# Performance work log

Measured on AMD Instinct MI355X. Metric: run time of the kernel, lower is better.

## Reference

```python
import math
import jax, jax.numpy as jnp
import numpy as np

HEADS = 8
D_MODEL = 256


def positional_encoding_2d(c, h, w):
    # faithful port of wzlxjtu/PositionalEncoding2D
    d = c // 2
    div_term = jnp.exp(jnp.arange(0.0, d, 2, dtype=jnp.float32) * (-(math.log(10000.0) / d)))  # [d//2? no: d/2 entries -> d//2]
    pos_w = jnp.arange(0.0, w, dtype=jnp.float32)[:, None] * div_term  # [w, d//2]
    pos_h = jnp.arange(0.0, h, dtype=jnp.float32)[:, None] * div_term  # [h, d//2]
    pe = jnp.zeros((c, h, w), dtype=jnp.float32)
    sw = jnp.broadcast_to(jnp.sin(pos_w).T[:, None, :], (div_term.shape[0], h, w))
    cw = jnp.broadcast_to(jnp.cos(pos_w).T[:, None, :], (div_term.shape[0], h, w))
    sh = jnp.broadcast_to(jnp.sin(pos_h).T[:, :, None], (div_term.shape[0], h, w))
    ch = jnp.broadcast_to(jnp.cos(pos_h).T[:, :, None], (div_term.shape[0], h, w))
    pe = pe.at[0:d:2].set(sw)
    pe = pe.at[1:d:2].set(cw)
    pe = pe.at[d::2].set(sh)
    pe = pe.at[d + 1::2].set(ch)
    return pe


def setup_inputs() -> dict:
    key = jax.random.key(0)
    ks = jax.random.split(key, 9)
    b, c, h, w = 2, D_MODEL, 64, 64
    x = jax.random.normal(ks[0], (b, c, h, w), dtype=jnp.float32)
    s = 0.02
    Wq = jax.random.normal(ks[1], (c, c), dtype=jnp.float32) * s
    Wk = jax.random.normal(ks[2], (c, c), dtype=jnp.float32) * s
    Wv = jax.random.normal(ks[3], (c, c), dtype=jnp.float32) * s
    Wo = jax.random.normal(ks[4], (c, c), dtype=jnp.float32) * s
    bq = jax.random.normal(ks[5], (c,), dtype=jnp.float32) * s
    bk = jax.random.normal(ks[6], (c,), dtype=jnp.float32) * s
    bv = jax.random.normal(ks[7], (c,), dtype=jnp.float32) * s
    bo = jax.random.normal(ks[8], (c,), dtype=jnp.float32) * s
    return {"x": x, "Wq": Wq, "bq": bq, "Wk": Wk, "bk": bk,
            "Wv": Wv, "bv": bv, "Wo": Wo, "bo": bo}


def reference(x, Wq, bq, Wk, bk, Wv, bv, Wo, bo):
    b, c, h, w = x.shape
    dk = c // HEADS
    pe = positional_encoding_2d(c, h, w)
    x2 = x + pe[None]                                   # [b,c,h,w]
    tok = x2.reshape(b, c, h * w).transpose(0, 2, 1)    # [b,N,c]
    q = (tok @ Wq.T + bq).reshape(b, -1, HEADS, dk).transpose(0, 2, 1, 3)  # [b,H,N,dk]
    k = (tok @ Wk.T + bk).reshape(b, -1, HEADS, dk).transpose(0, 2, 1, 3)
    v = (tok @ Wv.T + bv).reshape(b, -1, HEADS, dk).transpose(0, 2, 1, 3)
    scores = jnp.einsum('bhnd,bhmd->bhnm', q, k) / math.sqrt(dk)  # [b,H,N,N]
    attn = jax.nn.softmax(scores, axis=-1)
    out = jnp.einsum('bhnm,bhmd->bhnd', attn, v)        # [b,H,N,dk]
    concat = out.transpose(0, 2, 1, 3).reshape(b, -1, c)  # [b,N,c]
    proj = concat @ Wo.T + bo                           # [b,N,c]
    return proj.transpose(0, 2, 1).reshape(b, c, h, w)
```

## Files before the change

### kernel.cpp

```cpp
#include <hip/hip_runtime.h>
#include <hip/hip_bf16.h>
#include <cstdint>

typedef float f32x4 __attribute__((ext_vector_type(4)));
typedef __bf16 bf16x8 __attribute__((ext_vector_type(8)));
typedef __bf16 bf16x2 __attribute__((ext_vector_type(2)));
typedef uint32_t uint2v __attribute__((ext_vector_type(2)));
typedef uint32_t uint4v __attribute__((ext_vector_type(4)));

#define MFMA_K32(A, B, C) __builtin_amdgcn_mfma_f32_16x16x32_bf16((A), (B), (C), 0, 0, 0)

#if __has_builtin(__builtin_amdgcn_exp2f)
#define EXP2(x) __builtin_amdgcn_exp2f(x)
#else
#define EXP2(x) exp2f(x)
#endif

static __device__ __forceinline__ uint16_t f2b(float f) {
    uint32_t u = __float_as_uint(f);
    uint32_t r = (u + 0x7fffu + ((u >> 16) & 1u)) >> 16;
    return (uint16_t)r;
}

static __device__ __forceinline__ uint32_t packbf(float a, float b) {
#if __has_builtin(__builtin_amdgcn_cvt_pk_bf16_f32)
    bf16x2 v = __builtin_amdgcn_cvt_pk_bf16_f32(a, b);
    return *(uint32_t*)&v;
#else
    uint32_t ua = __float_as_uint(a);
    ua += 0x7fffu + ((ua >> 16) & 1u);
    uint32_t ub = __float_as_uint(b);
    ub += 0x7fffu + ((ub >> 16) & 1u);
    return __builtin_amdgcn_perm(ub, ua, 0x07060302);
#endif
}

__global__ __launch_bounds__(256) void peadd(const float* __restrict__ x,
                                             uint16_t* __restrict__ tok) {
    __shared__ uint16_t T[64][65];
    int t = threadIdx.x, bid = blockIdx.x;
    int nt = bid & 63, ct = (bid >> 6) & 3, bb = bid >> 8;
    int n0 = nt << 6, c0 = ct << 6;
    int nl = t & 63, cq = t >> 6;
    int n = n0 + nl;
    int posh = n0 >> 6;
    float pf = (float)((c0 & 128) ? posh : nl);
#pragma unroll
    for (int p = 0; p < 16; ++p) {
        int cl = cq * 16 + p;
        int cc = c0 + cl;
        int i = (cc & 127) >> 1;
        float dt = __expf((float)(2 * i) * -0.07195578415606394f);
        float sv, cv;
        __sincosf(pf * dt, &sv, &cv);
        float pe = (cc & 1) ? cv : sv;
        T[cl][nl] = f2b(x[((size_t)(bb * 256 + cc) << 12) + n] + pe);
    }
    __syncthreads();
#pragma unroll
    for (int p = 0; p < 16; ++p) {
        int tl = cq * 16 + p;
        tok[(((size_t)(bb << 12) | (n0 + tl)) << 8) + c0 + nl] = T[nl][tl];
    }
}

__global__ __launch_bounds__(256) void qkv_gemm(const uint16_t* __restrict__ tok,
                                                const float* __restrict__ wqp,
                                                const float* __restrict__ wkp,
                                                const float* __restrict__ wvp,
                                                const float* __restrict__ bq,
                                                const float* __restrict__ bk,
                                                const float* __restrict__ bv,
                                                uint16_t* __restrict__ qo,
                                                uint16_t* __restrict__ ko,
                                                uint16_t* __restrict__ vo) {
    __shared__ __align__(16) uint16_t WS[64][264];
    int tid = threadIdx.x, wv = tid >> 6, lane = tid & 63;
    int c16 = lane & 15, quad = lane >> 4;
    int M0 = blockIdx.x * 64 + wv * 16;
    int O0 = blockIdx.y * 64;
    const uint16_t* arow = tok + (size_t)(M0 + c16) * 256;
    bf16x8 af[8];
#pragma unroll
    for (int kk = 0; kk < 8; ++kk) af[kk] = *(const bf16x8*)(arow + kk * 32 + quad * 8);
    f32x4 zero = {0.f, 0.f, 0.f, 0.f};
    int bb = M0 >> 12, n = (M0 + c16) & 4095;
    int srow = tid >> 5, sch = (tid & 31) << 3;
    for (int mat = 0; mat < 3; ++mat) {
        const float* Wg = ((mat == 0) ? wqp : (mat == 1) ? wkp : wvp) + (size_t)O0 * 256;
        __syncthreads();
#pragma unroll
        for (int p = 0; p < 8; ++p) {
            const float* src = Wg + (size_t)(p * 8 + srow) * 256 + sch;
            f32x4 lo = *(const f32x4*)(src);
            f32x4 hi = *(const f32x4*)(src + 4);
            uint4v pk;
            pk[0] = packbf(lo[0], lo[1]);
            pk[1] = packbf(lo[2], lo[3]);
            pk[2] = packbf(hi[0], hi[1]);
            pk[3] = packbf(hi[2], hi[3]);
            *(uint4v*)(&WS[p * 8 + srow][sch]) = pk;
        }
        __syncthreads();
        f32x4 acc[4] = {zero, zero, zero, zero};
#pragma unroll
        for (int kk = 0; kk < 8; ++kk) {
            int k0 = kk * 32 + quad * 8;
#pragma unroll
            for (int nb = 0; nb < 4; ++nb)
                acc[nb] = MFMA_K32(*(const bf16x8*)(&WS[nb * 16 + c16][k0]),
                                   af[kk], acc[nb]);
        }
        const float* bias = (mat == 0) ? bq : (mat == 1) ? bk : bv;
        if (mat < 2) {
            float scale = (mat == 0) ? 0.25505654134660127f : 1.0f;
            uint16_t* dst = (mat == 0) ? qo : ko;
#pragma unroll
            for (int nb = 0; nb < 4; ++nb) {
                int o = O0 + nb * 16 + quad * 4;
                f32x4 bi = *(const f32x4*)(bias + o);
                int h = o >> 5, dd = o & 31;
                uint2v pk;
                pk[0] = packbf((acc[nb][0] + bi[0]) * scale, (acc[nb][1] + bi[1]) * scale);
                pk[1] = packbf((acc[nb][2] + bi[2]) * scale, (acc[nb][3] + bi[3]) * scale);
                *(uint2v*)(dst + ((size_t)(bb * 8 + h) * 4096 + n) * 32 + dd) = pk;
            }
        } else {
#pragma unroll
            for (int nb = 0; nb < 4; ++nb)
#pragma unroll
                for (int r = 0; r < 4; ++r) {
                    int o = O0 + nb * 16 + quad * 4 + r;
                    vo[((size_t)(bb * 8 + (o >> 5)) * 32 + (o & 31)) * 4096 + n] =
                        f2b(acc[nb][r] + bias[o]);
                }
        }
    }
}

__global__ __launch_bounds__(512, 4) void flash(const uint16_t* __restrict__ qb,
                                                const uint16_t* __restrict__ kb,
                                                const uint16_t* __restrict__ vtb,
                                                uint16_t* __restrict__ concat) {
    __shared__ __align__(16) char smem[38912];
    int tid = threadIdx.x, wv = tid >> 6, lane = tid & 63;
    int c16 = lane & 15, quad = lane >> 4;
    int half = tid >> 8, t2 = tid & 255;
    int bh = blockIdx.y;
    int q0 = (blockIdx.x << 7) + (wv & 3) * 32;
    size_t base = (size_t)bh << 12;

    uint16_t* KT = (uint16_t*)(smem + half * 19456);
    uint16_t* VT = (uint16_t*)(smem + half * 19456 + 10240);

    const uint16_t* kgp = kb + (base + (size_t)half * 2048 + (t2 >> 2)) * 32 + (t2 & 3) * 8;
    const uint16_t* vgp = vtb + ((size_t)bh * 32 + (t2 >> 3)) * 4096 + half * 2048 + (t2 & 7) * 8;
    uint16_t* kls = KT + (t2 >> 2) * 40 + (t2 & 3) * 8;
    uint16_t* vls = VT + (t2 >> 3) * 72 + (t2 & 7) * 8;

    bf16x8 qf0 = *(const bf16x8*)(qb + (base + q0 + c16) * 32 + quad * 8);
    bf16x8 qf1 = *(const bf16x8*)(qb + (base + q0 + 16 + c16) * 32 + quad * 8);

    int rbase = ((c16 >> 2) << 3) + (c16 & 3);

    union { uint32_t u[4]; bf16x8 v; } onesu;
    onesu.u[0] = 0x3F803F80u; onesu.u[1] = 0x3F803F80u;
    onesu.u[2] = 0x3F803F80u; onesu.u[3] = 0x3F803F80u;
    bf16x8 ones = onesu.v;

    f32x4 zero = {0.f, 0.f, 0.f, 0.f};
    f32x4 o00 = zero, o01 = zero, o10 = zero, o11 = zero;
    f32x4 oS0 = zero, oS1 = zero;

    {
        bf16x8 kr = *(const bf16x8*)kgp;
        bf16x8 vr = *(const bf16x8*)vgp;
        *(bf16x8*)kls = kr;
        *(bf16x8*)vls = vr;
    }
    __syncthreads();

    for (int kt = 0; kt < 32; ++kt) {
        int cur = kt & 1;
        int kn = (kt + 1) & 31;
        bf16x8 kr = *(const bf16x8*)(kgp + (size_t)kn * 2048);
        bf16x8 vr = *(const bf16x8*)(vgp + kn * 64);
        const uint16_t* kfp = KT + cur * 2560 + rbase * 40 + quad * 8;
        const uint16_t* vfp = VT + cur * 2304 + c16 * 72 + quad * 8;
        bf16x8 kf[4], vA[2], vB[2];
        kf[0] = *(const bf16x8*)(kfp);
        kf[1] = *(const bf16x8*)(kfp + 160);
        kf[2] = *(const bf16x8*)(kfp + 1280);
        kf[3] = *(const bf16x8*)(kfp + 1440);
        vA[0] = *(const bf16x8*)(vfp);
        vA[1] = *(const bf16x8*)(vfp + 32);
        vB[0] = *(const bf16x8*)(vfp + 1152);
        vB[1] = *(const bf16x8*)(vfp + 1152 + 32);

        f32x4 s0[4], s1[4];
#pragma unroll
        for (int c = 0; c < 4; ++c) s0[c] = MFMA_K32(kf[c], qf0, zero);
#pragma unroll
        for (int c = 0; c < 4; ++c) s1[c] = MFMA_K32(kf[c], qf1, zero);

#pragma unroll
        for (int p = 0; p < 2; ++p) {
#pragma unroll
            for (int r = 0; r < 4; ++r) {
                s0[2 * p][r] = EXP2(s0[2 * p][r]);
                s0[2 * p + 1][r] = EXP2(s0[2 * p + 1][r]);
                s1[2 * p][r] = EXP2(s1[2 * p][r]);
                s1[2 * p + 1][r] = EXP2(s1[2 * p + 1][r]);
            }
            union { bf16x8 v; uint32_t u[4]; } pa0, pa1;
            pa0.u[0] = packbf(s0[2 * p][0], s0[2 * p][1]);
            pa0.u[1] = packbf(s0[2 * p][2], s0[2 * p][3]);
            pa0.u[2] = packbf(s0[2 * p + 1][0], s0[2 * p + 1][1]);
            pa0.u[3] = packbf(s0[2 * p + 1][2], s0[2 * p + 1][3]);
            pa1.u[0] = packbf(s1[2 * p][0], s1[2 * p][1]);
            pa1.u[1] = packbf(s1[2 * p][2], s1[2 * p][3]);
            pa1.u[2] = packbf(s1[2 * p + 1][0], s1[2 * p + 1][1]);
            pa1.u[3] = packbf(s1[2 * p + 1][2], s1[2 * p + 1][3]);
            o00 = MFMA_K32(pa0.v, vA[p], o00);
            o01 = MFMA_K32(pa0.v, vB[p], o01);
            oS0 = MFMA_K32(pa0.v, ones, oS0);
            o10 = MFMA_K32(pa1.v, vA[p], o10);
            o11 = MFMA_K32(pa1.v, vB[p], o11);
            oS1 = MFMA_K32(pa1.v, ones, oS1);
        }

        *(bf16x8*)(kls + (cur ^ 1) * 2560) = kr;
        *(bf16x8*)(vls + (cur ^ 1) * 2304) = vr;
        __syncthreads();
    }

    float* ov = (float*)smem;
    if (wv >= 4) {
        float* d = ov + ((wv - 4) * 64 + lane) * 25;
#pragma unroll
        for (int r = 0; r < 4; ++r) {
            d[r] = o00[r]; d[4 + r] = o01[r]; d[8 + r] = o10[r]; d[12 + r] = o11[r];
            d[16 + r] = oS0[r]; d[20 + r] = oS1[r];
        }
    }
    __syncthreads();
    if (wv < 4) {
        const float* s = ov + (wv * 64 + lane) * 25;
#pragma unroll
        for (int r = 0; r < 4; ++r) {
            o00[r] += s[r]; o01[r] += s[4 + r]; o10[r] += s[8 + r]; o11[r] += s[12 + r];
            oS0[r] += s[16 + r]; oS1[r] += s[20 + r];
        }
        int h = bh & 7, bb = bh >> 3;
#pragma unroll
        for (int r = 0; r < 4; ++r) {
            float i0 = 1.f / oS0[r];
            float i1 = 1.f / oS1[r];
            int n = q0 + quad * 4 + r;
            size_t row0 = ((size_t)bb * 4096 + n) * 256 + h * 32;
            size_t row1 = ((size_t)bb * 4096 + n + 16) * 256 + h * 32;
            concat[row0 + c16]      = f2b(o00[r] * i0);
            concat[row0 + 16 + c16] = f2b(o01[r] * i0);
            concat[row1 + c16]      = f2b(o10[r] * i1);
            concat[row1 + 16 + c16] = f2b(o11[r] * i1);
        }
    }
}

__global__ __launch_bounds__(256) void proj_gemm(const uint16_t* __restrict__ concat,
                                                 const float* __restrict__ Wo,
                                                 const float* __restrict__ bo,
                                                 float* __restrict__ out) {
    __shared__ __align__(16) uint16_t WS[64][264];
    int tid = threadIdx.x, wv = tid >> 6, lane = tid & 63;
    int c16 = lane & 15, quad = lane >> 4;
    int M0 = blockIdx.x * 64 + wv * 16;
    int O0 = blockIdx.y * 64;
    int srow = tid >> 5, sch = (tid & 31) << 3;
    const float* Wg = Wo + (size_t)O0 * 256;
#pragma unroll
    for (int p = 0; p < 8; ++p) {
        const float* src = Wg + (size_t)(p * 8 + srow) * 256 + sch;
        f32x4 lo = *(const f32x4*)(src);
        f32x4 hi = *(const f32x4*)(src + 4);
        uint4v pk;
        pk[0] = packbf(lo[0], lo[1]);
        pk[1] = packbf(lo[2], lo[3]);
        pk[2] = packbf(hi[0], hi[1]);
        pk[3] = packbf(hi[2], hi[3]);
        *(uint4v*)(&WS[p * 8 + srow][sch]) = pk;
    }
    const uint16_t* crow = concat + (size_t)(M0 + c16) * 256;
    bf16x8 af[8];
#pragma unroll
    for (int kk = 0; kk < 8; ++kk) af[kk] = *(const bf16x8*)(crow + kk * 32 + quad * 8);
    __syncthreads();
    f32x4 zero = {0.f, 0.f, 0.f, 0.f};
    f32x4 acc[4] = {zero, zero, zero, zero};
#pragma unroll
    for (int kk = 0; kk < 8; ++kk) {
        int k0 = kk * 32 + quad * 8;
#pragma unroll
        for (int nb = 0; nb < 4; ++nb)
            acc[nb] = MFMA_K32(*(const bf16x8*)(&WS[nb * 16 + c16][k0]),
                               af[kk], acc[nb]);
    }
    int bb = M0 >> 12, n = (M0 + c16) & 4095;
#pragma unroll
    for (int nb = 0; nb < 4; ++nb)
#pragma unroll
        for (int r = 0; r < 4; ++r) {
            int o = O0 + nb * 16 + quad * 4 + r;
            out[((size_t)(bb * 256 + o) << 12) + n] = acc[nb][r] + bo[o];
        }
}

extern "C" void kernel_launch(void* const* d_in, const int* in_sizes, int n_in,
                              void* d_out, int out_size, void* d_ws, size_t ws_size,
                              hipStream_t stream) {
    const float* x  = (const float*)d_in[0];
    const float* Wq = (const float*)d_in[1];
    const float* bq = (const float*)d_in[2];
    const float* Wk = (const float*)d_in[3];
    const float* bk = (const float*)d_in[4];
    const float* Wv = (const float*)d_in[5];
    const float* bv = (const float*)d_in[6];
    const float* Wo = (const float*)d_in[7];
    const float* bo = (const float*)d_in[8];
    float* out = (float*)d_out;

    uint16_t* ws   = (uint16_t*)d_ws;
    uint16_t* tok  = ws;
    uint16_t* q    = tok + 2097152;
    uint16_t* k    = q + 2097152;
    uint16_t* vt   = k + 2097152;
    uint16_t* cc   = vt + 2097152;

    peadd<<<512, 256, 0, stream>>>(x, tok);
    qkv_gemm<<<dim3(128, 4), 256, 0, stream>>>(tok, Wq, Wk, Wv, bq, bk, bv, q, k, vt);
    flash<<<dim3(32, 16), 512, 0, stream>>>(q, k, vt, cc);
    proj_gemm<<<dim3(128, 4), 256, 0, stream>>>(cc, Wo, bo, out);
}
```

Measured before the change: 154.9 us.

## Fuse all four stages into one persistent kernel with grid barriers

Replaces the four separate launches (PE add, QKV GEMM, flash attention, output projection) with a single 512-block kernel. Stages are separated by atomic-counter grid barriers, and the barrier counters are zeroed with a memset each call. The aim is to remove inter-kernel launch gaps and tail effects. The PE-add stage now uses 512 threads and a recurrence for div_term, and the GEMM stages are re-tiled so 8 waves share one 64x64 tile. The barriers assume all 512 blocks are co-resident and add spin-wait cost; if the blocks cannot all be resident, the kernel deadlocks.

```diff
diff --git a/kernel.cpp b/kernel.cpp
--- a/kernel.cpp
+++ b/kernel.cpp
@@ -15,6 +15,8 @@
 #else
 #define EXP2(x) exp2f(x)
 #endif
+
+#define NBLK 512u
 
 static __device__ __forceinline__ uint16_t f2b(float f) {
     uint32_t u = __float_as_uint(f);
@@ -35,63 +37,263 @@
 #endif
 }
 
-__global__ __launch_bounds__(256) void peadd(const float* __restrict__ x,
-                                             uint16_t* __restrict__ tok) {
-    __shared__ uint16_t T[64][65];
-    int t = threadIdx.x, bid = blockIdx.x;
-    int nt = bid & 63, ct = (bid >> 6) & 3, bb = bid >> 8;
-    int n0 = nt << 6, c0 = ct << 6;
-    int nl = t & 63, cq = t >> 6;
-    int n = n0 + nl;
-    int posh = n0 >> 6;
-    float pf = (float)((c0 & 128) ? posh : nl);
-#pragma unroll
-    for (int p = 0; p < 16; ++p) {
-        int cl = cq * 16 + p;
-        int cc = c0 + cl;
-        int i = (cc & 127) >> 1;
-        float dt = __expf((float)(2 * i) * -0.07195578415606394f);
-        float sv, cv;
-        __sincosf(pf * dt, &sv, &cv);
-        float pe = (cc & 1) ? cv : sv;
-        T[cl][nl] = f2b(x[((size_t)(bb * 256 + cc) << 12) + n] + pe);
-    }
+static __device__ __forceinline__ void gridbar(unsigned* cnt) {
     __syncthreads();
-#pragma unroll
-    for (int p = 0; p < 16; ++p) {
-        int tl = cq * 16 + p;
-        tok[(((size_t)(bb << 12) | (n0 + tl)) << 8) + c0 + nl] = T[nl][tl];
-    }
-}
-
-__global__ __launch_bounds__(256) void qkv_gemm(const uint16_t* __restrict__ tok,
-                                                const float* __restrict__ wqp,
-                                                const float* __restrict__ wkp,
-                                                const float* __restrict__ wvp,
-                                                const float* __restrict__ bq,
-                                                const float* __restrict__ bk,
-                                                const float* __restrict__ bv,
-                                                uint16_t* __restrict__ qo,
-                                                uint16_t* __restrict__ ko,
-                                                uint16_t* __restrict__ vo) {
-    __shared__ __align__(16) uint16_t WS[64][264];
-    int tid = threadIdx.x, wv = tid >> 6, lane = tid & 63;
+    if (threadIdx.x == 0) {
+        __threadfence();
+        __hip_atomic_fetch_add(cnt, 1u, __ATOMIC_RELEASE, __HIP_MEMORY_SCOPE_AGENT);
+        while (__hip_atomic_load(cnt, __ATOMIC_ACQUIRE, __HIP_MEMORY_SCOPE_AGENT) < NBLK)
+            __builtin_amdgcn_s_sleep(2);
+        __threadfence();
+    }
+    __syncthreads();
+}
+
+__global__ __launch_bounds__(512, 4) void fused(
+        const float* __restrict__ x,
+        const float* __restrict__ wqp, const float* __restrict__ bq,
+        const float* __restrict__ wkp, const float* __restrict__ bk,
+        const float* __restrict__ wvp, const float* __restrict__ bv,
+        const float* __restrict__ wop, const float* __restrict__ bo,
+        uint16_t* __restrict__ tok, uint16_t* __restrict__ qg,
+        uint16_t* __restrict__ kg, uint16_t* __restrict__ vtg,
+        uint16_t* __restrict__ ccg, float* __restrict__ out,
+        unsigned* __restrict__ bar) {
+    __shared__ __align__(16) char smem[38912];
+    int tid = threadIdx.x, bid = blockIdx.x;
+    int wv = tid >> 6, lane = tid & 63;
     int c16 = lane & 15, quad = lane >> 4;
-    int M0 = blockIdx.x * 64 + wv * 16;
-    int O0 = blockIdx.y * 64;
-    const uint16_t* arow = tok + (size_t)(M0 + c16) * 256;
-    bf16x8 af[8];
-#pragma unroll
-    for (int kk = 0; kk < 8; ++kk) af[kk] = *(const bf16x8*)(arow + kk * 32 + quad * 8);
     f32x4 zero = {0.f, 0.f, 0.f, 0.f};
-    int bb = M0 >> 12, n = (M0 + c16) & 4095;
-    int srow = tid >> 5, sch = (tid & 31) << 3;
-    for (int mat = 0; mat < 3; ++mat) {
-        const float* Wg = ((mat == 0) ? wqp : (mat == 1) ? wkp : wvp) + (size_t)O0 * 256;
+
+    {
+        uint16_t(*T)[65] = (uint16_t(*)[65])smem;
+        int nt = bid & 63, ct = (bid >> 6) & 3, bb = bid >> 8;
+        int n0 = nt << 6, c0 = ct << 6;
+        int nl = tid & 63, cq = tid >> 6;
+        int n = n0 + nl;
+        float pf = (float)((c0 & 128) ? nt : nl);
+        int cbase = c0 + cq * 8;
+        int ibase = (cbase & 127) >> 1;
+        float dt = __expf((float)(2 * ibase) * -0.07195578415606394f);
+#pragma unroll
+        for (int j = 0; j < 4; ++j) {
+            float sv, cv;
+            __sincosf(pf * dt, &sv, &cv);
+            int cl = cq * 8 + 2 * j;
+            int cc = cbase + 2 * j;
+            T[cl][nl]     = f2b(x[((size_t)(bb * 256 + cc) << 12) + n] + sv);
+            T[cl + 1][nl] = f2b(x[((size_t)(bb * 256 + cc + 1) << 12) + n] + cv);
+            dt *= 0.8659643233600653f;
+        }
         __syncthreads();
 #pragma unroll
         for (int p = 0; p < 8; ++p) {
-            const float* src = Wg + (size_t)(p * 8 + srow) * 256 + sch;
+            int tl = cq * 8 + p;
+            tok[(((size_t)(bb << 12) | (n0 + tl)) << 8) + c0 + nl] = T[nl][tl];
+        }
+    }
+    gridbar(bar + 0);
+
+    {
+        uint16_t(*WS)[264] = (uint16_t(*)[264])smem;
+        int mtile = bid & 127, otile = bid >> 7;
+        int M0 = mtile * 64 + (wv & 3) * 16;
+        int obase = otile * 64 + (wv >> 2) * 32;
+        int wr = (wv >> 2) * 32;
+        const uint16_t* arow = tok + (size_t)(M0 + c16) * 256;
+        bf16x8 af[8];
+#pragma unroll
+        for (int kk = 0; kk < 8; ++kk) af[kk] = *(const bf16x8*)(arow + kk * 32 + quad * 8);
+        int bb = M0 >> 12, n = (M0 + c16) & 4095;
+        int srow = tid >> 5, sch = (tid & 31) << 3;
+        for (int mat = 0; mat < 3; ++mat) {
+            const float* Wg = ((mat == 0) ? wqp : (mat == 1) ? wkp : wvp)
+                              + (size_t)(otile * 64) * 256;
+            __syncthreads();
+#pragma unroll
+            for (int p = 0; p < 4; ++p) {
+                const float* src = Wg + (size_t)(p * 16 + srow) * 256 + sch;
+                f32x4 lo = *(const f32x4*)(src);
+                f32x4 hi = *(const f32x4*)(src + 4);
+                uint4v pk;
+                pk[0] = packbf(lo[0], lo[1]);
+                pk[1] = packbf(lo[2], lo[3]);
+                pk[2] = packbf(hi[0], hi[1]);
+                pk[3] = packbf(hi[2], hi[3]);
+                *(uint4v*)(&WS[p * 16 + srow][sch]) = pk;
+            }
+            __syncthreads();
+            f32x4 acc[2] = {zero, zero};
+#pragma unroll
+            for (int kk = 0; kk < 8; ++kk) {
+                int k0 = kk * 32 + quad * 8;
+#pragma unroll
+                for (int nb = 0; nb < 2; ++nb)
+                    acc[nb] = MFMA_K32(*(const bf16x8*)(&WS[wr + nb * 16 + c16][k0]),
+                                       af[kk], acc[nb]);
+            }
+            const float* bias = (mat == 0) ? bq : (mat == 1) ? bk : bv;
+            if (mat < 2) {
+                float scale = (mat == 0) ? 0.25505654134660127f : 1.0f;
+                uint16_t* dst = (mat == 0) ? qg : kg;
+#pragma unroll
+                for (int nb = 0; nb < 2; ++nb) {
+                    int o = obase + nb * 16 + quad * 4;
+                    f32x4 bi = *(const f32x4*)(bias + o);
+                    int h = o >> 5, dd = o & 31;
+                    uint2v pk;
+                    pk[0] = packbf((acc[nb][0] + bi[0]) * scale, (acc[nb][1] + bi[1]) * scale);
+                    pk[1] = packbf((acc[nb][2] + bi[2]) * scale, (acc[nb][3] + bi[3]) * scale);
+                    *(uint2v*)(dst + ((size_t)(bb * 8 + h) * 4096 + n) * 32 + dd) = pk;
+                }
+            } else {
+#pragma unroll
+                for (int nb = 0; nb < 2; ++nb)
+#pragma unroll
+                    for (int r = 0; r < 4; ++r) {
+                        int o = obase + nb * 16 + quad * 4 + r;
+                        vtg[((size_t)(bb * 8 + (o >> 5)) * 32 + (o & 31)) * 4096 + n] =
+                            f2b(acc[nb][r] + bias[o]);
+                    }
+            }
+        }
+    }
+    gridbar(bar + 1);
+
+    {
+        int qt = bid & 31, bh = bid >> 5;
+        int half = tid >> 8, t2 = tid & 255;
+        int q0 = (qt << 7) + (wv & 3) * 32;
+        size_t base = (size_t)bh << 12;
+
+        uint16_t* KT = (uint16_t*)(smem + half * 19456);
+        uint16_t* VT = (uint16_t*)(smem + half * 19456 + 10240);
+
+        const uint16_t* kgp = kg + (base + (size_t)half * 2048 + (t2 >> 2)) * 32 + (t2 & 3) * 8;
+        const uint16_t* vgp = vtg + ((size_t)bh * 32 + (t2 >> 3)) * 4096 + half * 2048 + (t2 & 7) * 8;
+        uint16_t* kls = KT + (t2 >> 2) * 40 + (t2 & 3) * 8;
+        uint16_t* vls = VT + (t2 >> 3) * 72 + (t2 & 7) * 8;
+
+        bf16x8 qf0 = *(const bf16x8*)(qg + (base + q0 + c16) * 32 + quad * 8);
+        bf16x8 qf1 = *(const bf16x8*)(qg + (base + q0 + 16 + c16) * 32 + quad * 8);
+
+        int rbase = ((c16 >> 2) << 3) + (c16 & 3);
+
+        union { uint32_t u[4]; bf16x8 v; } onesu;
+        onesu.u[0] = 0x3F803F80u; onesu.u[1] = 0x3F803F80u;
+        onesu.u[2] = 0x3F803F80u; onesu.u[3] = 0x3F803F80u;
+        bf16x8 ones = onesu.v;
+
+        f32x4 o00 = zero, o01 = zero, o10 = zero, o11 = zero;
+        f32x4 oS0 = zero, oS1 = zero;
+
+        {
+            bf16x8 kr = *(const bf16x8*)kgp;
+            bf16x8 vr = *(const bf16x8*)vgp;
+            *(bf16x8*)kls = kr;
+            *(bf16x8*)vls = vr;
+        }
+        __syncthreads();
+
+        for (int kt = 0; kt < 32; ++kt) {
+            int cur = kt & 1;
+            int kn = (kt + 1) & 31;
+            bf16x8 kr = *(const bf16x8*)(kgp + (size_t)kn * 2048);
+            bf16x8 vr = *(const bf16x8*)(vgp + kn * 64);
+            const uint16_t* kfp = KT + cur * 2560 + rbase * 40 + quad * 8;
+            const uint16_t* vfp = VT + cur * 2304 + c16 * 72 + quad * 8;
+            bf16x8 kf[4], vA[2], vB[2];
+            kf[0] = *(const bf16x8*)(kfp);
+            kf[1] = *(const bf16x8*)(kfp + 160);
+            kf[2] = *(const bf16x8*)(kfp + 1280);
+            kf[3] = *(const bf16x8*)(kfp + 1440);
+            vA[0] = *(const bf16x8*)(vfp);
+            vA[1] = *(const bf16x8*)(vfp + 32);
+            vB[0] = *(const bf16x8*)(vfp + 1152);
+            vB[1] = *(const bf16x8*)(vfp + 1152 + 32);
+
+            f32x4 s0[4], s1[4];
+#pragma unroll
+            for (int c = 0; c < 4; ++c) s0[c] = MFMA_K32(kf[c], qf0, zero);
+#pragma unroll
+            for (int c = 0; c < 4; ++c) s1[c] = MFMA_K32(kf[c], qf1, zero);
+
+#pragma unroll
+            for (int p = 0; p < 2; ++p) {
+#pragma unroll
+                for (int r = 0; r < 4; ++r) {
+                    s0[2 * p][r] = EXP2(s0[2 * p][r]);
+                    s0[2 * p + 1][r] = EXP2(s0[2 * p + 1][r]);
+                    s1[2 * p][r] = EXP2(s1[2 * p][r]);
+                    s1[2 * p + 1][r] = EXP2(s1[2 * p + 1][r]);
+                }
+                union { bf16x8 v; uint32_t u[4]; } pa0, pa1;
+                pa0.u[0] = packbf(s0[2 * p][0], s0[2 * p][1]);
+                pa0.u[1] = packbf(s0[2 * p][2], s0[2 * p][3]);
+                pa0.u[2] = packbf(s0[2 * p + 1][0], s0[2 * p + 1][1]);
+                pa0.u[3] = packbf(s0[2 * p + 1][2], s0[2 * p + 1][3]);
+                pa1.u[0] = packbf(s1[2 * p][0], s1[2 * p][1]);
+                pa1.u[1] = packbf(s1[2 * p][2], s1[2 * p][3]);
+                pa1.u[2] = packbf(s1[2 * p + 1][0], s1[2 * p + 1][1]);
+                pa1.u[3] = packbf(s1[2 * p + 1][2], s1[2 * p + 1][3]);
+                o00 = MFMA_K32(pa0.v, vA[p], o00);
+                o01 = MFMA_K32(pa0.v, vB[p], o01);
+                oS0 = MFMA_K32(pa0.v, ones, oS0);
+                o10 = MFMA_K32(pa1.v, vA[p], o10);
+                o11 = MFMA_K32(pa1.v, vB[p], o11);
+                oS1 = MFMA_K32(pa1.v, ones, oS1);
+            }
+
+            *(bf16x8*)(kls + (cur ^ 1) * 2560) = kr;
+            *(bf16x8*)(vls + (cur ^ 1) * 2304) = vr;
+            __syncthreads();
+        }
+
+        float* ov = (float*)smem;
+        if (wv >= 4) {
+            float* d = ov + ((wv - 4) * 64 + lane) * 25;
+#pragma unroll
+            for (int r = 0; r < 4; ++r) {
+                d[r] = o00[r]; d[4 + r] = o01[r]; d[8 + r] = o10[r]; d[12 + r] = o11[r];
+                d[16 + r] = oS0[r]; d[20 + r] = oS1[r];
+            }
+        }
+        __syncthreads();
+        if (wv < 4) {
+            const float* s = ov + (wv * 64 + lane) * 25;
+#pragma unroll
+            for (int r = 0; r < 4; ++r) {
+                o00[r] += s[r]; o01[r] += s[4 + r]; o10[r] += s[8 + r]; o11[r] += s[12 + r];
+                oS0[r] += s[16 + r]; oS1[r] += s[20 + r];
+            }
+            int h = bh & 7, bb = bh >> 3;
+#pragma unroll
+            for (int r = 0; r < 4; ++r) {
+                float i0 = 1.f / oS0[r];
+                float i1 = 1.f / oS1[r];
+                int n = q0 + quad * 4 + r;
+                size_t row0 = ((size_t)bb * 4096 + n) * 256 + h * 32;
+                size_t row1 = ((size_t)bb * 4096 + n + 16) * 256 + h * 32;
+                ccg[row0 + c16]      = f2b(o00[r] * i0);
+                ccg[row0 + 16 + c16] = f2b(o01[r] * i0);
+                ccg[row1 + c16]      = f2b(o10[r] * i1);
+                ccg[row1 + 16 + c16] = f2b(o11[r] * i1);
+            }
+        }
+    }
+    gridbar(bar + 2);
+
+    {
+        uint16_t(*WS)[264] = (uint16_t(*)[264])smem;
+        int mtile = bid & 127, otile = bid >> 7;
+        int M0 = mtile * 64 + (wv & 3) * 16;
+        int obase = otile * 64 + (wv >> 2) * 32;
+        int wr = (wv >> 2) * 32;
+        int srow = tid >> 5, sch = (tid & 31) << 3;
+        const float* Wg = wop + (size_t)(otile * 64) * 256;
+#pragma unroll
+        for (int p = 0; p < 4; ++p) {
+            const float* src = Wg + (size_t)(p * 16 + srow) * 256 + sch;
             f32x4 lo = *(const f32x4*)(src);
             f32x4 hi = *(const f32x4*)(src + 4);
             uint4v pk;
@@ -99,220 +301,31 @@
             pk[1] = packbf(lo[2], lo[3]);
             pk[2] = packbf(hi[0], hi[1]);
             pk[3] = packbf(hi[2], hi[3]);
-            *(uint4v*)(&WS[p * 8 + srow][sch]) = pk;
-        }
+            *(uint4v*)(&WS[p * 16 + srow][sch]) = pk;
+        }
+        const uint16_t* crow = ccg + (size_t)(M0 + c16) * 256;
+        bf16x8 af[8];
+#pragma unroll
+        for (int kk = 0; kk < 8; ++kk) af[kk] = *(const bf16x8*)(crow + kk * 32 + quad * 8);
         __syncthreads();
-        f32x4 acc[4] = {zero, zero, zero, zero};
+        f32x4 acc[2] = {zero, zero};
 #pragma unroll
         for (int kk = 0; kk < 8; ++kk) {
             int k0 = kk * 32 + quad * 8;
 #pragma unroll
-            for (int nb = 0; nb < 4; ++nb)
-                acc[nb] = MFMA_K32(*(const bf16x8*)(&WS[nb * 16 + c16][k0]),
+            for (int nb = 0; nb < 2; ++nb)
+                acc[nb] = MFMA_K32(*(const bf16x8*)(&WS[wr + nb * 16 + c16][k0]),
                                    af[kk], acc[nb]);
         }
-        const float* bias = (mat == 0) ? bq : (mat == 1) ? bk : bv;
-        if (mat < 2) {
-            float scale = (mat == 0) ? 0.25505654134660127f : 1.0f;
-            uint16_t* dst = (mat == 0) ? qo : ko;
-#pragma unroll
-            for (int nb = 0; nb < 4; ++nb) {
-                int o = O0 + nb * 16 + quad * 4;
-                f32x4 bi = *(const f32x4*)(bias + o);
-                int h = o >> 5, dd = o & 31;
-                uint2v pk;
-                pk[0] = packbf((acc[nb][0] + bi[0]) * scale, (acc[nb][1] + bi[1]) * scale);
-                pk[1] = packbf((acc[nb][2] + bi[2]) * scale, (acc[nb][3] + bi[3]) * scale);
-                *(uint2v*)(dst + ((size_t)(bb * 8 + h) * 4096 + n) * 32 + dd) = pk;
-            }
-        } else {
-#pragma unroll
-            for (int nb = 0; nb < 4; ++nb)
-#pragma unroll
-                for (int r = 0; r < 4; ++r) {
-                    int o = O0 + nb * 16 + quad * 4 + r;
-                    vo[((size_t)(bb * 8 + (o >> 5)) * 32 + (o & 31)) * 4096 + n] =
-                        f2b(acc[nb][r] + bias[o]);
-                }
-        }
-    }
-}
-
-__global__ __launch_bounds__(512, 4) void flash(const uint16_t* __restrict__ qb,
-                                                const uint16_t* __restrict__ kb,
-                                                const uint16_t* __restrict__ vtb,
-                                                uint16_t* __restrict__ concat) {
-    __shared__ __align__(16) char smem[38912];
-    int tid = threadIdx.x, wv = tid >> 6, lane = tid & 63;
-    int c16 = lane & 15, quad = lane >> 4;
-    int half = tid >> 8, t2 = tid & 255;
-    int bh = blockIdx.y;
-    int q0 = (blockIdx.x << 7) + (wv & 3) * 32;
-    size_t base = (size_t)bh << 12;
-
-    uint16_t* KT = (uint16_t*)(smem + half * 19456);
-    uint16_t* VT = (uint16_t*)(smem + half * 19456 + 10240);
-
-    const uint16_t* kgp = kb + (base + (size_t)half * 2048 + (t2 >> 2)) * 32 + (t2 & 3) * 8;
-    const uint16_t* vgp = vtb + ((size_t)bh * 32 + (t2 >> 3)) * 4096 + half * 2048 + (t2 & 7) * 8;
-    uint16_t* kls = KT + (t2 >> 2) * 40 + (t2 & 3) * 8;
-    uint16_t* vls = VT + (t2 >> 3) * 72 + (t2 & 7) * 8;
-
-    bf16x8 qf0 = *(const bf16x8*)(qb + (base + q0 + c16) * 32 + quad * 8);
-    bf16x8 qf1 = *(const bf16x8*)(qb + (base + q0 + 16 + c16) * 32 + quad * 8);
-
-    int rbase = ((c16 >> 2) << 3) + (c16 & 3);
-
-    union { uint32_t u[4]; bf16x8 v; } onesu;
-    onesu.u[0] = 0x3F803F80u; onesu.u[1] = 0x3F803F80u;
-    onesu.u[2] = 0x3F803F80u; onesu.u[3] = 0x3F803F80u;
-    bf16x8 ones = onesu.v;
-
-    f32x4 zero = {0.f, 0.f, 0.f, 0.f};
-    f32x4 o00 = zero, o01 = zero, o10 = zero, o11 = zero;
-    f32x4 oS0 = zero, oS1 = zero;
-
-    {
-        bf16x8 kr = *(const bf16x8*)kgp;
-        bf16x8 vr = *(const bf16x8*)vgp;
-        *(bf16x8*)kls = kr;
-        *(bf16x8*)vls = vr;
-    }
-    __syncthreads();
-
-    for (int kt = 0; kt < 32; ++kt) {
-        int cur = kt & 1;
-        int kn = (kt + 1) & 31;
-        bf16x8 kr = *(const bf16x8*)(kgp + (size_t)kn * 2048);
-        bf16x8 vr = *(const bf16x8*)(vgp + kn * 64);
-        const uint16_t* kfp = KT + cur * 2560 + rbase * 40 + quad * 8;
-        const uint16_t* vfp = VT + cur * 2304 + c16 * 72 + quad * 8;
-        bf16x8 kf[4], vA[2], vB[2];
-        kf[0] = *(const bf16x8*)(kfp);
-        kf[1] = *(const bf16x8*)(kfp + 160);
-        kf[2] = *(const bf16x8*)(kfp + 1280);
-        kf[3] = *(const bf16x8*)(kfp + 1440);
-        vA[0] = *(const bf16x8*)(vfp);
-        vA[1] = *(const bf16x8*)(vfp + 32);
-        vB[0] = *(const bf16x8*)(vfp + 1152);
-        vB[1] = *(const bf16x8*)(vfp + 1152 + 32);
-
-        f32x4 s0[4], s1[4];
-#pragma unroll
-        for (int c = 0; c < 4; ++c) s0[c] = MFMA_K32(kf[c], qf0, zero);
-#pragma unroll
-        for (int c = 0; c < 4; ++c) s1[c] = MFMA_K32(kf[c], qf1, zero);
-
-#pragma unroll
-        for (int p = 0; p < 2; ++p) {
+        int bb = M0 >> 12, n = (M0 + c16) & 4095;
+#pragma unroll
+        for (int nb = 0; nb < 2; ++nb)
 #pragma unroll
             for (int r = 0; r < 4; ++r) {
-                s0[2 * p][r] = EXP2(s0[2 * p][r]);
-                s0[2 * p + 1][r] = EXP2(s0[2 * p + 1][r]);
-                s1[2 * p][r] = EXP2(s1[2 * p][r]);
-                s1[2 * p + 1][r] = EXP2(s1[2 * p + 1][r]);
-            }
-            union { bf16x8 v; uint32_t u[4]; } pa0, pa1;
-            pa0.u[0] = packbf(s0[2 * p][0], s0[2 * p][1]);
-            pa0.u[1] = packbf(s0[2 * p][2], s0[2 * p][3]);
-            pa0.u[2] = packbf(s0[2 * p + 1][0], s0[2 * p + 1][1]);
-            pa0.u[3] = packbf(s0[2 * p + 1][2], s0[2 * p + 1][3]);
-            pa1.u[0] = packbf(s1[2 * p][0], s1[2 * p][1]);
-            pa1.u[1] = packbf(s1[2 * p][2], s1[2 * p][3]);
-            pa1.u[2] = packbf(s1[2 * p + 1][0], s1[2 * p + 1][1]);
-            pa1.u[3] = packbf(s1[2 * p + 1][2], s1[2 * p + 1][3]);
-            o00 = MFMA_K32(pa0.v, vA[p], o00);
-            o01 = MFMA_K32(pa0.v, vB[p], o01);
-            oS0 = MFMA_K32(pa0.v, ones, oS0);
-            o10 = MFMA_K32(pa1.v, vA[p], o10);
-            o11 = MFMA_K32(pa1.v, vB[p], o11);
-            oS1 = MFMA_K32(pa1.v, ones, oS1);
-        }
-
-        *(bf16x8*)(kls + (cur ^ 1) * 2560) = kr;
-        *(bf16x8*)(vls + (cur ^ 1) * 2304) = vr;
-        __syncthreads();
-    }
-
-    float* ov = (float*)smem;
-    if (wv >= 4) {
-        float* d = ov + ((wv - 4) * 64 + lane) * 25;
-#pragma unroll
-        for (int r = 0; r < 4; ++r) {
-            d[r] = o00[r]; d[4 + r] = o01[r]; d[8 + r] = o10[r]; d[12 + r] = o11[r];
-            d[16 + r] = oS0[r]; d[20 + r] = oS1[r];
-        }
-    }
-    __syncthreads();
-    if (wv < 4) {
-        const float* s = ov + (wv * 64 + lane) * 25;
-#pragma unroll
-        for (int r = 0; r < 4; ++r) {
-            o00[r] += s[r]; o01[r] += s[4 + r]; o10[r] += s[8 + r]; o11[r] += s[12 + r];
-            oS0[r] += s[16 + r]; oS1[r] += s[20 + r];
-        }
-        int h = bh & 7, bb = bh >> 3;
-#pragma unroll
-        for (int r = 0; r < 4; ++r) {
-            float i0 = 1.f / oS0[r];
-            float i1 = 1.f / oS1[r];
-            int n = q0 + quad * 4 + r;
-            size_t row0 = ((size_t)bb * 4096 + n) * 256 + h * 32;
-            size_t row1 = ((size_t)bb * 4096 + n + 16) * 256 + h * 32;
-            concat[row0 + c16]      = f2b(o00[r] * i0);
-            concat[row0 + 16 + c16] = f2b(o01[r] * i0);
-            concat[row1 + c16]      = f2b(o10[r] * i1);
-            concat[row1 + 16 + c16] = f2b(o11[r] * i1);
-        }
-    }
-}
-
-__global__ __launch_bounds__(256) void proj_gemm(const uint16_t* __restrict__ concat,
-                                                 const float* __restrict__ Wo,
-                                                 const float* __restrict__ bo,
-                                                 float* __restrict__ out) {
-    __shared__ __align__(16) uint16_t WS[64][264];
-    int tid = threadIdx.x, wv = tid >> 6, lane = tid & 63;
-    int c16 = lane & 15, quad = lane >> 4;
-    int M0 = blockIdx.x * 64 + wv * 16;
-    int O0 = blockIdx.y * 64;
-    int srow = tid >> 5, sch = (tid & 31) << 3;
-    const float* Wg = Wo + (size_t)O0 * 256;
-#pragma unroll
-    for (int p = 0; p < 8; ++p) {
-        const float* src = Wg + (size_t)(p * 8 + srow) * 256 + sch;
-        f32x4 lo = *(const f32x4*)(src);
-        f32x4 hi = *(const f32x4*)(src + 4);
-        uint4v pk;
-        pk[0] = packbf(lo[0], lo[1]);
-        pk[1] = packbf(lo[2], lo[3]);
-        pk[2] = packbf(hi[0], hi[1]);
-        pk[3] = packbf(hi[2], hi[3]);
-        *(uint4v*)(&WS[p * 8 + srow][sch]) = pk;
-    }
-    const uint16_t* crow = concat + (size_t)(M0 + c16) * 256;
-    bf16x8 af[8];
-#pragma unroll
-    for (int kk = 0; kk < 8; ++kk) af[kk] = *(const bf16x8*)(crow + kk * 32 + quad * 8);
-    __syncthreads();
-    f32x4 zero = {0.f, 0.f, 0.f, 0.f};
-    f32x4 acc[4] = {zero, zero, zero, zero};
-#pragma unroll
-    for (int kk = 0; kk < 8; ++kk) {
-        int k0 = kk * 32 + quad * 8;
-#pragma unroll
-        for (int nb = 0; nb < 4; ++nb)
-            acc[nb] = MFMA_K32(*(const bf16x8*)(&WS[nb * 16 + c16][k0]),
-                               af[kk], acc[nb]);
-    }
-    int bb = M0 >> 12, n = (M0 + c16) & 4095;
-#pragma unroll
-    for (int nb = 0; nb < 4; ++nb)
-#pragma unroll
-        for (int r = 0; r < 4; ++r) {
-            int o = O0 + nb * 16 + quad * 4 + r;
-            out[((size_t)(bb * 256 + o) << 12) + n] = acc[nb][r] + bo[o];
-        }
+                int o = obase + nb * 16 + quad * 4 + r;
+                out[((size_t)(bb * 256 + o) << 12) + n] = acc[nb][r] + bo[o];
+            }
+    }
 }
 
 extern "C" void kernel_launch(void* const* d_in, const int* in_sizes, int n_in,
@@ -335,9 +348,9 @@
     uint16_t* k    = q + 2097152;
     uint16_t* vt   = k + 2097152;
     uint16_t* cc   = vt + 2097152;
-
-    peadd<<<512, 256, 0, stream>>>(x, tok);
-    qkv_gemm<<<dim3(128, 4), 256, 0, stream>>>(tok, Wq, Wk, Wv, bq, bk, bv, q, k, vt);
-    flash<<<dim3(32, 16), 512, 0, stream>>>(q, k, vt, cc);
-    proj_gemm<<<dim3(128, 4), 256, 0, stream>>>(cc, Wo, bo, out);
-}
+    unsigned* bar  = (unsigned*)(cc + 2097152);
+
+    hipMemsetAsync((void*)bar, 0, 16, stream);
+    fused<<<512, 512, 0, stream>>>(x, Wq, bq, Wk, bk, Wv, bv, Wo, bo,
+                                   tok, q, k, vt, cc, out, bar);
+}
```

After: 431.7 us. 179% more time.
